# Performance work log

Hardware: AMD Instinct MI355X
Metric: run time of the kernel (lower is better)

Reference implementation:

```python
import jax, jax.numpy as jnp
import numpy as np

NUM_VALUES = 1048576   # rows in the source value store
NUM_WEIGHTS = 65536    # unique learned weight matrices (deduplicated)
E = 4194304            # total (neuron, input) edges across the layer
DIN = 8
DOUT = 8


def setup_inputs() -> dict:
    key = jax.random.key(0)
    k1, k2, k3, k4 = jax.random.split(key, 4)
    values = jax.random.normal(k1, (NUM_VALUES, DIN), dtype=jnp.float32)
    weights = jax.random.normal(k2, (NUM_WEIGHTS, DOUT, DIN), dtype=jnp.float32)
    input_idx = jax.random.randint(k3, (E,), 0, NUM_VALUES, dtype=jnp.int32)
    weight_idx = jax.random.randint(k4, (E,), 0, NUM_WEIGHTS, dtype=jnp.int32)
    return {"values": values, "weights": weights,
            "input_idx": input_idx, "weight_idx": weight_idx}


def reference(values, weights, input_idx, weight_idx):
    # self.gather(layer_values): gather activations by precomputed ordinals
    x = jnp.take(values, input_idx, axis=0)          # [E, DIN]
    # self.gather_weights(w): gather (possibly shared) weight matrices
    w = jnp.take(weights, weight_idx, axis=0)        # [E, DOUT, DIN]
    # y = w @ input_values  (per-edge dense matmul)
    y = jnp.einsum('eoi,ei->eo', w, x)               # [E, DOUT]
    return y
```

## Files before the change

kernel.cpp:

```cpp
#include <hip/hip_runtime.h>
#include <hip/hip_bf16.h>
#include <stdint.h>


__device__ __forceinline__ float bflo(uint32_t u) {
    union { uint32_t u; float f; } c; c.u = u << 16; return c.f;
}
__device__ __forceinline__ float bfhi(uint32_t u) {
    union { uint32_t u; float f; } c; c.u = u & 0xffff0000u; return c.f;
}

__global__ __launch_bounds__(256) void convert_weights_kernel(
    const float4* __restrict__ src,
    ushort4*      __restrict__ dst,
    int n4)
{
    int i = blockIdx.x * blockDim.x + threadIdx.x;
    if (i >= n4) return;
    float4 v = src[i];
    ushort4 r;
    r.x = __bfloat16_as_ushort(__float2bfloat16(v.x));
    r.y = __bfloat16_as_ushort(__float2bfloat16(v.y));
    r.z = __bfloat16_as_ushort(__float2bfloat16(v.z));
    r.w = __bfloat16_as_ushort(__float2bfloat16(v.w));
    dst[i] = r;
}

__global__ __launch_bounds__(256) void edge_linear_bf16w_kernel(
    const float*    __restrict__ values,
    const uint32_t* __restrict__ wbf,
    const int*      __restrict__ input_idx,
    const int*      __restrict__ weight_idx,
    float*          __restrict__ out,
    int E)
{
    int gid = blockIdx.x * blockDim.x + threadIdx.x;
    int e = gid >> 3;
    if (e >= E) return;
    int o = gid & 7;

    int iidx = input_idx[e];
    int widx = weight_idx[e];

    const float4* xp = (const float4*)(values + (size_t)iidx * 8u);
    const uint4*  wp = (const uint4*)(wbf + (size_t)widx * 32u + (uint32_t)o * 4u);

    uint4  wv = *wp;
    float4 x0 = xp[0];
    float4 x1 = xp[1];

    float acc = 0.0f;
    acc = fmaf(bflo(wv.x), x0.x, acc);
    acc = fmaf(bfhi(wv.x), x0.y, acc);
    acc = fmaf(bflo(wv.y), x0.z, acc);
    acc = fmaf(bfhi(wv.y), x0.w, acc);
    acc = fmaf(bflo(wv.z), x1.x, acc);
    acc = fmaf(bfhi(wv.z), x1.y, acc);
    acc = fmaf(bflo(wv.w), x1.z, acc);
    acc = fmaf(bfhi(wv.w), x1.w, acc);

    out[gid] = acc;
}

__global__ __launch_bounds__(256) void edge_linear_f32_kernel(
    const float* __restrict__ values,
    const float* __restrict__ weights,
    const int*   __restrict__ input_idx,
    const int*   __restrict__ weight_idx,
    float*       __restrict__ out,
    int E)
{
    int gid = blockIdx.x * blockDim.x + threadIdx.x;
    int e = gid >> 3;
    if (e >= E) return;
    int o = gid & 7;
    int iidx = input_idx[e];
    int widx = weight_idx[e];
    const float4* xp = (const float4*)(values  + (size_t)iidx * 8u);
    const float4* wp = (const float4*)(weights + (size_t)widx * 64u + (uint32_t)o * 8u);
    float4 x0 = xp[0], x1 = xp[1], w0 = wp[0], w1 = wp[1];
    float acc = 0.0f;
    acc = fmaf(w0.x, x0.x, acc); acc = fmaf(w0.y, x0.y, acc);
    acc = fmaf(w0.z, x0.z, acc); acc = fmaf(w0.w, x0.w, acc);
    acc = fmaf(w1.x, x1.x, acc); acc = fmaf(w1.y, x1.y, acc);
    acc = fmaf(w1.z, x1.z, acc); acc = fmaf(w1.w, x1.w, acc);
    out[gid] = acc;
}

extern "C" void kernel_launch(void* const* d_in, const int* in_sizes, int n_in,
                              void* d_out, int out_size, void* d_ws, size_t ws_size,
                              hipStream_t stream) {
    const float* values     = (const float*)d_in[0];
    const float* weights    = (const float*)d_in[1];
    const int*   input_idx  = (const int*)d_in[2];
    const int*   weight_idx = (const int*)d_in[3];
    float*       out        = (float*)d_out;

    int E  = in_sizes[2];
    int NW = in_sizes[1];
    size_t need = (size_t)NW * sizeof(uint16_t);

    long long threads = (long long)E * 8;
    int block = 256;
    int grid = (int)((threads + block - 1) / block);

    if (ws_size >= need) {
        int n4 = NW / 4;
        int cgrid = (n4 + 255) / 256;
        convert_weights_kernel<<<cgrid, 256, 0, stream>>>(
            (const float4*)weights, (ushort4*)d_ws, n4);
        edge_linear_bf16w_kernel<<<grid, block, 0, stream>>>(
            values, (const uint32_t*)d_ws, input_idx, weight_idx, out, E);
    } else {
        edge_linear_f32_kernel<<<grid, block, 0, stream>>>(
            values, weights, input_idx, weight_idx, out, E);
    }
}
```

Baseline: 314.4 us.

## Split edge kernel into two weight-range passes and use nontemporal loads/stores

Launches the edge kernel with twice the blocks. Each half handles only edges whose weight index falls in one half of the weight table, so the bf16 weight working set per pass is smaller and more likely to stay cache-resident. Streaming index loads, value gathers, the output store and the weight conversion are marked nontemporal so they do not evict cached weights. The cost is that the indices are read twice, half the threads in each pass exit early, and edges are processed in scattered order.

```diff
diff --git a/kernel.cpp b/kernel.cpp
--- a/kernel.cpp
+++ b/kernel.cpp
@@ -2,6 +2,10 @@
 #include <hip/hip_bf16.h>
 #include <stdint.h>
 
+
+typedef float          f32x4 __attribute__((ext_vector_type(4)));
+typedef unsigned int   u32x4 __attribute__((ext_vector_type(4)));
+typedef unsigned short u16x4 __attribute__((ext_vector_type(4)));
 
 __device__ __forceinline__ float bflo(uint32_t u) {
     union { uint32_t u; float f; } c; c.u = u << 16; return c.f;
@@ -11,43 +15,48 @@
 }
 
 __global__ __launch_bounds__(256) void convert_weights_kernel(
-    const float4* __restrict__ src,
-    ushort4*      __restrict__ dst,
+    const f32x4* __restrict__ src,
+    u16x4*       __restrict__ dst,
     int n4)
 {
     int i = blockIdx.x * blockDim.x + threadIdx.x;
     if (i >= n4) return;
-    float4 v = src[i];
-    ushort4 r;
+    f32x4 v = __builtin_nontemporal_load(&src[i]);
+    u16x4 r;
     r.x = __bfloat16_as_ushort(__float2bfloat16(v.x));
     r.y = __bfloat16_as_ushort(__float2bfloat16(v.y));
     r.z = __bfloat16_as_ushort(__float2bfloat16(v.z));
     r.w = __bfloat16_as_ushort(__float2bfloat16(v.w));
-    dst[i] = r;
+    __builtin_nontemporal_store(r, &dst[i]);
 }
 
-__global__ __launch_bounds__(256) void edge_linear_bf16w_kernel(
+__global__ __launch_bounds__(256) void edge_linear_bf16w_2pass_kernel(
     const float*    __restrict__ values,
     const uint32_t* __restrict__ wbf,
     const int*      __restrict__ input_idx,
     const int*      __restrict__ weight_idx,
     float*          __restrict__ out,
-    int E)
+    int E, int blocksPerPass, int wThresh)
 {
-    int gid = blockIdx.x * blockDim.x + threadIdx.x;
+    int pass = (blockIdx.x >= (unsigned)blocksPerPass) ? 1 : 0;
+    int bx   = blockIdx.x - pass * blocksPerPass;
+    int gid  = bx * blockDim.x + threadIdx.x;
     int e = gid >> 3;
     if (e >= E) return;
     int o = gid & 7;
 
-    int iidx = input_idx[e];
-    int widx = weight_idx[e];
+    int widx = __builtin_nontemporal_load(&weight_idx[e]);
+    int p = (widx >= wThresh) ? 1 : 0;
+    if (p != pass) return;
 
-    const float4* xp = (const float4*)(values + (size_t)iidx * 8u);
-    const uint4*  wp = (const uint4*)(wbf + (size_t)widx * 32u + (uint32_t)o * 4u);
+    int iidx = __builtin_nontemporal_load(&input_idx[e]);
 
-    uint4  wv = *wp;
-    float4 x0 = xp[0];
-    float4 x1 = xp[1];
+    const f32x4* xp = (const f32x4*)(values + (size_t)iidx * 8u);
+    const u32x4* wp = (const u32x4*)(wbf + (size_t)widx * 32u + (uint32_t)o * 4u);
+
+    u32x4 wv = *wp;
+    f32x4 x0 = __builtin_nontemporal_load(xp);
+    f32x4 x1 = __builtin_nontemporal_load(xp + 1);
 
     float acc = 0.0f;
     acc = fmaf(bflo(wv.x), x0.x, acc);
@@ -59,7 +68,7 @@
     acc = fmaf(bflo(wv.w), x1.z, acc);
     acc = fmaf(bfhi(wv.w), x1.w, acc);
 
-    out[gid] = acc;
+    __builtin_nontemporal_store(acc, &out[gid]);
 }
 
 __global__ __launch_bounds__(256) void edge_linear_f32_kernel(
@@ -102,17 +111,20 @@
 
     long long threads = (long long)E * 8;
     int block = 256;
-    int grid = (int)((threads + block - 1) / block);
+    int blocksPerPass = (int)((threads + block - 1) / block);
 
     if (ws_size >= need) {
         int n4 = NW / 4;
         int cgrid = (n4 + 255) / 256;
         convert_weights_kernel<<<cgrid, 256, 0, stream>>>(
-            (const float4*)weights, (ushort4*)d_ws, n4);
-        edge_linear_bf16w_kernel<<<grid, block, 0, stream>>>(
-            values, (const uint32_t*)d_ws, input_idx, weight_idx, out, E);
+            (const f32x4*)weights, (u16x4*)d_ws, n4);
+        int numW   = NW / 64;
+        int wThresh = numW >> 1;
+        edge_linear_bf16w_2pass_kernel<<<blocksPerPass * 2, block, 0, stream>>>(
+            values, (const uint32_t*)d_ws, input_idx, weight_idx, out,
+            E, blocksPerPass, wThresh);
     } else {
-        edge_linear_f32_kernel<<<grid, block, 0, stream>>>(
+        edge_linear_f32_kernel<<<blocksPerPass, block, 0, stream>>>(
             values, weights, input_idx, weight_idx, out, E);
     }
 }
```

After: 476.0 us. +51.4%, slower.
